# Kernel tuning notes

Hardware: AMD Instinct MI355X
Metric: run time of the kernel (lower is better)

The kernel has to match this reference:

```python
import jax, jax.numpy as jnp
import numpy as np

CHANNELS = [64, 128, 256, 512, 512]
RES = [256, 128, 64, 32, 16]
N = 8          # batch
NQ = 128       # n_quad
NCW = 128      # nc_w (output descriptor size)
GRAD_BOOST = 10.0


def _norm(x):
    # Norm module: per-sample, per-row normalization over last dim; torch std is unbiased (ddof=1)
    m = jnp.mean(x, axis=-1, keepdims=True)
    s = jnp.std(x, axis=-1, ddof=1, keepdims=True)
    return (x - m) / (s + 1e-8)


def _quad(x, w):
    # Quad_module: (M^T @ softmax(grad_boost*w, axis=0))**2, summed over spatial dim
    n, c, h, wd = x.shape
    M = x.reshape(n, c, h * wd)                      # (N, C, HW)
    sm = jax.nn.softmax(w * GRAD_BOOST, axis=0)      # (C, NQ)
    proj = jnp.einsum('nch,co->nho', M, sm)          # (N, HW, NQ)
    return jnp.sum(proj ** 2, axis=1)                # (N, NQ)


def setup_inputs() -> dict:
    key = jax.random.key(0)
    ks = jax.random.split(key, 20)
    inp = {}
    for i, (c, r) in enumerate(zip(CHANNELS, RES)):
        inp[f"x{i}"] = jax.random.normal(ks[i], (N, c, r, r), dtype=jnp.float32)
        # torch init: 5/grad_boost * rand(n_in, n_out) = 0.5 * U[0,1)
        inp[f"w1_{i}"] = 0.5 * jax.random.uniform(ks[5 + i], (c, NQ), dtype=jnp.float32)
    d_in = len(CHANNELS) * NQ
    inp["fc1_w"] = jax.random.normal(ks[10], (d_in, 512), dtype=jnp.float32) * 0.04
    inp["fc1_b"] = jnp.zeros((512,), dtype=jnp.float32)
    inp["fc2_w"] = jax.random.normal(ks[11], (512, 512), dtype=jnp.float32) * 0.04
    inp["fc2_b"] = jnp.zeros((512,), dtype=jnp.float32)
    inp["fc3_w"] = jax.random.normal(ks[12], (512, NCW), dtype=jnp.float32) * 0.04
    inp["fc3_b"] = jnp.zeros((NCW,), dtype=jnp.float32)
    return inp


def reference(x0, x1, x2, x3, x4, w1_0, w1_1, w1_2, w1_3, w1_4,
              fc1_w, fc1_b, fc2_w, fc2_b, fc3_w, fc3_b):
    xs = [x0, x1, x2, x3, x4]
    ws = [w1_0, w1_1, w1_2, w1_3, w1_4]
    feats = [_norm(_quad(x, w)) for x, w in zip(xs, ws)]  # each (N, NQ)
    h = jnp.concatenate(feats, axis=1)                    # (N, 5*NQ)
    h = jax.nn.leaky_relu(_norm(h @ fc1_w + fc1_b), 0.01)
    h = jax.nn.leaky_relu(_norm(h @ fc2_w + fc2_b), 0.01)
    return h @ fc3_w + fc3_b                              # (N, NCW)
```

## Files before the change

### kernel.cpp

```cpp
#include <hip/hip_runtime.h>
#include <hip/hip_bf16.h>
#include <stdint.h>

#define NQ 128
#define NLVL 5

typedef float  floatx4 __attribute__((ext_vector_type(4)));
typedef short  short8  __attribute__((ext_vector_type(8)));

__device__ __forceinline__ uint16_t f2bf(float f) {
    uint32_t u = __builtin_bit_cast(uint32_t, f);
    uint32_t r = u + 0x7FFFu + ((u >> 16) & 1u);
    return (uint16_t)(r >> 16);
}
__device__ __forceinline__ uint32_t pack2(float a, float b) {
    return (uint32_t)f2bf(a) | ((uint32_t)f2bf(b) << 16);
}
__device__ __forceinline__ float bf2f(uint16_t u) {
    return __builtin_bit_cast(float, (uint32_t)u << 16);
}

struct SmParams {
    const float* w[NLVL];
    uint16_t*    smT[NLVL];
    int          C[NLVL];
};

__global__ __launch_bounds__(64) void softmax_kernel(SmParams p) {
    int b   = blockIdx.x;
    int lvl = b >> 7;
    int o   = b & 127;
    int C   = p.C[lvl];
    const float* w = p.w[lvl];
    int lane = threadIdx.x;
    float ev[8];
    int nIter = C >> 6;
    float mx = -1e30f;
    for (int it = 0; it < nIter; ++it) {
        float z = 10.0f * w[(size_t)(it * 64 + lane) * NQ + o];
        ev[it] = z;
        mx = fmaxf(mx, z);
    }
    #pragma unroll
    for (int s = 32; s; s >>= 1) mx = fmaxf(mx, __shfl_xor(mx, s));
    float sum = 0.f;
    for (int it = 0; it < nIter; ++it) { ev[it] = expf(ev[it] - mx); sum += ev[it]; }
    #pragma unroll
    for (int s = 32; s; s >>= 1) sum += __shfl_xor(sum, s);
    float inv = 1.0f / sum;
    uint16_t* dst = p.smT[lvl] + (size_t)o * C;
    for (int it = 0; it < nIter; ++it) dst[it * 64 + lane] = f2bf(ev[it] * inv);
}

struct GramParams { const float* x0; const float* x1; float* g0; float* g1; };

template<int C, int HW, int NS>
__device__ __forceinline__ void gram_body(const float* __restrict__ xb,
                                          float* __restrict__ gb,
                                          int h0, short* lds) {
    constexpr int RF   = C / 64;
    constexpr int CF   = C / 16;
    constexpr int PASS = C / 16;
    constexpr int STR  = 72;

    int t    = threadIdx.x;
    int wv   = t >> 6, lane = t & 63, m = lane & 15, kg = lane >> 4;
    int rrow = t >> 4;
    int rcol = (t & 15) * 4;
    const float* src = xb + (size_t)rrow * HW + rcol + h0;

    floatx4 acc[RF][CF];
    floatx4 zero = {0.f, 0.f, 0.f, 0.f};
    #pragma unroll
    for (int rf = 0; rf < RF; ++rf)
        #pragma unroll
        for (int cf = 0; cf < CF; ++cf) acc[rf][cf] = zero;

    float4 pf[PASS];
    #pragma unroll
    for (int p = 0; p < PASS; ++p) pf[p] = *(const float4*)(src + (size_t)p * 16 * HW);
    #pragma unroll
    for (int p = 0; p < PASS; ++p) {
        uint2 pk = { pack2(pf[p].x, pf[p].y), pack2(pf[p].z, pf[p].w) };
        *(uint2*)&lds[(p * 16 + rrow) * STR + rcol] = pk;
    }

    int cur = 0;
    for (int s = 0; s < NS; ++s) {
        if (s + 1 < NS) {
            const float* s2 = src + (s + 1) * 64;
            #pragma unroll
            for (int p = 0; p < PASS; ++p) pf[p] = *(const float4*)(s2 + (size_t)p * 16 * HW);
        }
        __syncthreads();
        const short* bc = lds + cur * (C * STR);
        #pragma unroll
        for (int ksl = 0; ksl < 2; ++ksl) {
            short8 fr[CF], af[RF];
            #pragma unroll
            for (int f = 0; f < CF; ++f)
                fr[f] = *(const short8*)&bc[(f * 16 + m) * STR + ksl * 32 + kg * 8];
            #pragma unroll
            for (int rf = 0; rf < RF; ++rf)
                af[rf] = *(const short8*)&bc[((wv * RF + rf) * 16 + m) * STR + ksl * 32 + kg * 8];
            #pragma unroll
            for (int rf = 0; rf < RF; ++rf)
                #pragma unroll
                for (int cf = 0; cf < CF; ++cf)
                    acc[rf][cf] = __builtin_amdgcn_mfma_f32_16x16x32_bf16(
                        af[rf], fr[cf], acc[rf][cf], 0, 0, 0);
        }
        if (s + 1 < NS) {
            short* bn = lds + (cur ^ 1) * (C * STR);
            #pragma unroll
            for (int p = 0; p < PASS; ++p) {
                uint2 pk = { pack2(pf[p].x, pf[p].y), pack2(pf[p].z, pf[p].w) };
                *(uint2*)&bn[(p * 16 + rrow) * STR + rcol] = pk;
            }
        }
        cur ^= 1;
    }

    #pragma unroll
    for (int rf = 0; rf < RF; ++rf) {
        int row0 = (wv * RF + rf) * 16 + kg * 4;
        #pragma unroll
        for (int cf = 0; cf < CF; ++cf) {
            int col = cf * 16 + m;
            #pragma unroll
            for (int r = 0; r < 4; ++r)
                atomicAdd(&gb[(size_t)(row0 + r) * C + col], acc[rf][cf][r]);
        }
    }
}

__global__ __launch_bounds__(256) void gram_kernel(GramParams p) {
    __shared__ __align__(16) short lds[2 * 128 * 72];
    int b = blockIdx.x;
    if (b < 512) {
        int n = b >> 6, ch = b & 63;
        gram_body<64, 65536, 16>(p.x0 + (size_t)n * 64 * 65536,
                                 p.g0 + (size_t)n * 64 * 64, ch * 1024, lds);
    } else {
        int b2 = b - 512;
        int n = b2 >> 5, ch = b2 & 31;
        gram_body<128, 16384, 8>(p.x1 + (size_t)n * 128 * 16384,
                                 p.g1 + (size_t)n * 128 * 128, ch * 512, lds);
    }
}

struct SgsParams {
    const float* g0; const float* g1;
    const uint16_t* smT0; const uint16_t* smT1;
    float* quad;
};

template<int C>
__device__ __forceinline__ void sgs_body(const float* __restrict__ g,
                                         const uint16_t* __restrict__ smT,
                                         float* __restrict__ qdst, short* Gt) {
    constexpr int RF  = C / 64;
    constexpr int KSL = C / 32;
    constexpr int STR = C + 8;
    int t = threadIdx.x;
    short* Ghi = Gt;
    short* Glo = Gt + C * STR;
    for (int i = t; i < C * C / 4; i += 256) {
        int row = i / (C / 4);
        int c4  = (i % (C / 4)) * 4;
        float4 v = *(const float4*)(g + (size_t)row * C + c4);
        uint16_t h0 = f2bf(v.x), h1 = f2bf(v.y), h2 = f2bf(v.z), h3 = f2bf(v.w);
        uint2 ph = { (uint32_t)h0 | ((uint32_t)h1 << 16),
                     (uint32_t)h2 | ((uint32_t)h3 << 16) };
        uint2 pl = { pack2(v.x - bf2f(h0), v.y - bf2f(h1)),
                     pack2(v.z - bf2f(h2), v.w - bf2f(h3)) };
        *(uint2*)&Ghi[row * STR + c4] = ph;
        *(uint2*)&Glo[row * STR + c4] = pl;
    }
    __syncthreads();
    int wv = t >> 6, lane = t & 63, m = lane & 15, kg = lane >> 4;
    floatx4 acc[RF][8];
    floatx4 zero = {0.f, 0.f, 0.f, 0.f};
    #pragma unroll
    for (int rf = 0; rf < RF; ++rf)
        #pragma unroll
        for (int ot = 0; ot < 8; ++ot) acc[rf][ot] = zero;

    #pragma unroll
    for (int ksl = 0; ksl < KSL; ++ksl) {
        short8 bf[8];
        #pragma unroll
        for (int ot = 0; ot < 8; ++ot)
            bf[ot] = *(const short8*)(smT + (size_t)(ot * 16 + m) * C + ksl * 32 + kg * 8);
        #pragma unroll
        for (int rf = 0; rf < RF; ++rf) {
            int roff = ((wv * RF + rf) * 16 + m) * STR + ksl * 32 + kg * 8;
            short8 ah = *(const short8*)&Ghi[roff];
            short8 al = *(const short8*)&Glo[roff];
            #pragma unroll
            for (int ot = 0; ot < 8; ++ot) {
                acc[rf][ot] = __builtin_amdgcn_mfma_f32_16x16x32_bf16(ah, bf[ot], acc[rf][ot], 0, 0, 0);
                acc[rf][ot] = __builtin_amdgcn_mfma_f32_16x16x32_bf16(al, bf[ot], acc[rf][ot], 0, 0, 0);
            }
        }
    }
    #pragma unroll
    for (int ot = 0; ot < 8; ++ot) {
        float part = 0.f;
        #pragma unroll
        for (int rf = 0; rf < RF; ++rf) {
            int c0 = (wv * RF + rf) * 16 + kg * 4;
            #pragma unroll
            for (int r = 0; r < 4; ++r) {
                float sv = bf2f(smT[(size_t)(ot * 16 + m) * C + c0 + r]);
                part = fmaf(sv, acc[rf][ot][r], part);
            }
        }
        part += __shfl_xor(part, 16);
        part += __shfl_xor(part, 32);
        if (lane < 16) atomicAdd(qdst + (size_t)(ot * 16 + lane) * 16, part);
    }
}

__global__ __launch_bounds__(256) void sgs_kernel(SgsParams p) {
    __shared__ __align__(16) short Gt[2 * 128 * 136];
    int b = blockIdx.x, lvl = b >> 3, n = b & 7;
    if (lvl == 0)
        sgs_body<64>(p.g0 + (size_t)n * 64 * 64, p.smT0,
                     p.quad + (size_t)n * 128 * 16, Gt);
    else
        sgs_body<128>(p.g1 + (size_t)n * 128 * 128, p.smT1,
                      p.quad + (size_t)(8 + n) * 128 * 16, Gt);
}

struct QuadParams {
    const float*    x[NLVL];
    const uint16_t* smT[NLVL];
    float*          quad;
    int             C[NLVL];
    int             HW[NLVL];
    int             blk_base[NLVL];
};

__global__ __launch_bounds__(256) void quad_kernel(QuadParams p) {
    __shared__ __align__(16) short At[64 * 40];
    __shared__ __align__(16) short Bt[128 * 40];

    int bid = blockIdx.x;
    int lvl = 0;
    #pragma unroll
    for (int l = 1; l < 3; ++l) if (bid >= p.blk_base[l]) lvl = l;
    int rel = bid - p.blk_base[lvl];
    int n   = rel & 7;
    int ht  = rel >> 3;
    int C   = p.C[lvl];
    int HW  = p.HW[lvl];
    int h0  = ht * 64;

    const float*    xb  = p.x[lvl] + (size_t)n * C * HW + h0;
    const uint16_t* smT = p.smT[lvl];

    int t    = threadIdx.x;
    int wave = t >> 6;
    int lane = t & 63;
    int m    = lane & 15;
    int kg   = lane >> 4;

    floatx4 acc[4][2];
    floatx4 zero = {0.f, 0.f, 0.f, 0.f};
    #pragma unroll
    for (int i = 0; i < 4; ++i)
        #pragma unroll
        for (int j = 0; j < 2; ++j) acc[i][j] = zero;

    int c_l = (t & 15) * 2;
    int h_l = (t >> 4) * 4;

    for (int c0 = 0; c0 < C; c0 += 32) {
        const float* s1 = xb + (size_t)(c0 + c_l) * HW + h_l;
        float4 a4 = *(const float4*)s1;
        float4 b4 = *(const float4*)(s1 + HW);
        #pragma unroll
        for (int j = 0; j < 4; ++j) {
            uint32_t pk = (uint32_t)f2bf(((const float*)&a4)[j]) |
                          ((uint32_t)f2bf(((const float*)&b4)[j]) << 16);
            *(uint32_t*)&At[(h_l + j) * 40 + c_l] = pk;
        }
        #pragma unroll
        for (int it = 0; it < 2; ++it) {
            int idx  = it * 256 + t;
            int o    = idx >> 2;
            int part = idx & 3;
            uint4 v = *(const uint4*)(smT + (size_t)o * C + c0 + part * 8);
            *(uint4*)&Bt[o * 40 + part * 8] = v;
        }
        __syncthreads();

        short8 af[4];
        #pragma unroll
        for (int mt = 0; mt < 4; ++mt)
            af[mt] = *(const short8*)&At[(mt * 16 + m) * 40 + kg * 8];
        short8 bfr[2];
        #pragma unroll
        for (int ot = 0; ot < 2; ++ot)
            bfr[ot] = *(const short8*)&Bt[((wave * 2 + ot) * 16 + m) * 40 + kg * 8];
        #pragma unroll
        for (int mt = 0; mt < 4; ++mt)
            #pragma unroll
            for (int ot = 0; ot < 2; ++ot)
                acc[mt][ot] = __builtin_amdgcn_mfma_f32_16x16x32_bf16(
                    af[mt], bfr[ot], acc[mt][ot], 0, 0, 0);
        __syncthreads();
    }

    float* qbase = p.quad + (size_t)((lvl + 2) * 8 + n) * 128 * 16;
    #pragma unroll
    for (int ot = 0; ot < 2; ++ot) {
        float part = 0.f;
        #pragma unroll
        for (int mt = 0; mt < 4; ++mt)
            #pragma unroll
            for (int r = 0; r < 4; ++r) {
                float v = acc[mt][ot][r];
                part = fmaf(v, v, part);
            }
        part += __shfl_xor(part, 16);
        part += __shfl_xor(part, 32);
        if (lane < 16) {
            int o = (wave * 2 + ot) * 16 + lane;
            atomicAdd(qbase + (size_t)o * 16, part);
        }
    }
}


__global__ __launch_bounds__(256) void hfc1_kernel(
    const float* __restrict__ quad, const float* __restrict__ w,
    const float* __restrict__ b, float* __restrict__ h1) {
    __shared__ float feat[640];
    __shared__ float stats[10];
    __shared__ float part[256];
    int blk = blockIdx.x;
    int n = blk >> 3, c8 = blk & 7;
    int t = threadIdx.x;
    for (int idx = t; idx < 640; idx += 256) {
        int L = idx >> 7, o = idx & 127;
        feat[idx] = quad[((size_t)(L * 8 + n) * 128 + o) * 16];
    }
    __syncthreads();
    int wv = t >> 6, lane = t & 63;
    for (int L = wv; L < 5; L += 4) {
        float a = feat[L * 128 + lane], c = feat[L * 128 + 64 + lane];
        float s = a + c;
        #pragma unroll
        for (int sh = 32; sh; sh >>= 1) s += __shfl_xor(s, sh);
        float mean = s * (1.f / 128.f);
        float d0 = a - mean, d1 = c - mean;
        float v = d0 * d0 + d1 * d1;
        #pragma unroll
        for (int sh = 32; sh; sh >>= 1) v += __shfl_xor(v, sh);
        if (lane == 0) {
            stats[L]     = mean;
            stats[5 + L] = 1.f / (sqrtf(v * (1.f / 127.f)) + 1e-8f);
        }
    }
    __syncthreads();
    for (int idx = t; idx < 640; idx += 256) {
        int L = idx >> 7;
        feat[idx] = (feat[idx] - stats[L]) * stats[5 + L];
    }
    __syncthreads();

    int o = c8 * 64 + lane;
    float acc = 0.f;
    const float* wc = w + o;
    int k0 = wv * 160;
    #pragma unroll 8
    for (int k = k0; k < k0 + 160; ++k) acc = fmaf(feat[k], wc[(size_t)k * 512], acc);
    part[t] = acc;
    __syncthreads();
    if (t < 64) {
        float r = part[t] + part[t + 64] + part[t + 128] + part[t + 192];
        h1[(size_t)n * 512 + c8 * 64 + t] = r + b[c8 * 64 + t];
    }
}

__device__ __forceinline__ void norm_leaky_512(float* buf, float* red, int t) {
    float a = buf[t], c = buf[t + 256];
    float s = a + c;
    #pragma unroll
    for (int sh = 32; sh; sh >>= 1) s += __shfl_xor(s, sh);
    if ((t & 63) == 0) red[t >> 6] = s;
    __syncthreads();
    float mean = (red[0] + red[1] + red[2] + red[3]) * (1.f / 512.f);
    float d0 = a - mean, d1 = c - mean;
    float v = d0 * d0 + d1 * d1;
    #pragma unroll
    for (int sh = 32; sh; sh >>= 1) v += __shfl_xor(v, sh);
    __syncthreads();
    if ((t & 63) == 0) red[t >> 6] = v;
    __syncthreads();
    float inv = 1.f / (sqrtf((red[0] + red[1] + red[2] + red[3]) * (1.f / 511.f)) + 1e-8f);
    float n0 = d0 * inv, n1 = d1 * inv;
    buf[t]       = n0 > 0.f ? n0 : 0.01f * n0;
    buf[t + 256] = n1 > 0.f ? n1 : 0.01f * n1;
    __syncthreads();
}

__global__ __launch_bounds__(256) void hfc2_kernel(
    const float* __restrict__ h1, const float* __restrict__ w,
    const float* __restrict__ b, float* __restrict__ h2) {
    __shared__ float buf[512];
    __shared__ float red[4];
    __shared__ float part[256];
    int blk = blockIdx.x;
    int n = blk >> 3, c8 = blk & 7;
    int t = threadIdx.x;
    buf[t]       = h1[(size_t)n * 512 + t];
    buf[t + 256] = h1[(size_t)n * 512 + t + 256];
    __syncthreads();
    norm_leaky_512(buf, red, t);
    int wv = t >> 6, lane = t & 63;
    int o = c8 * 64 + lane;
    float acc = 0.f;
    const float* wc = w + o;
    int k0 = wv * 128;
    #pragma unroll 8
    for (int k = k0; k < k0 + 128; ++k) acc = fmaf(buf[k], wc[(size_t)k * 512], acc);
    part[t] = acc;
    __syncthreads();
    if (t < 64) {
        float r = part[t] + part[t + 64] + part[t + 128] + part[t + 192];
        h2[(size_t)n * 512 + c8 * 64 + t] = r + b[c8 * 64 + t];
    }
}

__global__ __launch_bounds__(256) void hfc3_kernel(
    const float* __restrict__ h2, const float* __restrict__ w,
    const float* __restrict__ b, float* __restrict__ out) {
    __shared__ float buf[512];
    __shared__ float red[4];
    __shared__ float part[256];
    int blk = blockIdx.x;
    int n = blk >> 1, c2 = blk & 1;
    int t = threadIdx.x;
    buf[t]       = h2[(size_t)n * 512 + t];
    buf[t + 256] = h2[(size_t)n * 512 + t + 256];
    __syncthreads();
    norm_leaky_512(buf, red, t);
    int wv = t >> 6, lane = t & 63;
    int o = c2 * 64 + lane;
    float acc = 0.f;
    const float* wc = w + o;
    int k0 = wv * 128;
    #pragma unroll 8
    for (int k = k0; k < k0 + 128; ++k) acc = fmaf(buf[k], wc[(size_t)k * 128], acc);
    part[t] = acc;
    __syncthreads();
    if (t < 64) {
        out[(size_t)n * 128 + c2 * 64 + t] =
            part[t] + part[t + 64] + part[t + 128] + part[t + 192] + b[c2 * 64 + t];
    }
}

extern "C" void kernel_launch(void* const* d_in, const int* in_sizes, int n_in,
                              void* d_out, int out_size, void* d_ws, size_t ws_size,
                              hipStream_t stream) {
    static const int Cs[NLVL]   = {64, 128, 256, 512, 512};
    static const int RESs[NLVL] = {256, 128, 64, 32, 16};

    const float* x[NLVL];
    const float* w[NLVL];
    for (int i = 0; i < NLVL; ++i) {
        x[i] = (const float*)d_in[2 * i];
        w[i] = (const float*)d_in[2 * i + 1];
    }
    const float* fc1_w = (const float*)d_in[10];
    const float* fc1_b = (const float*)d_in[11];
    const float* fc2_w = (const float*)d_in[12];
    const float* fc2_b = (const float*)d_in[13];
    const float* fc3_w = (const float*)d_in[14];
    const float* fc3_b = (const float*)d_in[15];

    uint16_t* smT_base = (uint16_t*)d_ws;
    int smOff[NLVL];
    int off = 0;
    for (int i = 0; i < NLVL; ++i) { smOff[i] = off; off += Cs[i] * NQ; }
    size_t smBytes = (size_t)off * sizeof(uint16_t);
    float* quad = (float*)((char*)d_ws + smBytes);
    size_t quadFloats = (size_t)NLVL * 8 * NQ * 16;
    float* g0 = quad + quadFloats;
    float* g1 = g0 + (size_t)8 * 64 * 64;
    float* h1 = g1 + (size_t)8 * 128 * 128;
    float* h2 = h1 + (size_t)8 * 512;
    size_t zeroBytes = (quadFloats + (size_t)8 * 64 * 64 + (size_t)8 * 128 * 128) * sizeof(float);

    SmParams sp;
    for (int i = 0; i < NLVL; ++i) {
        sp.w[i]   = w[i];
        sp.smT[i] = smT_base + smOff[i];
        sp.C[i]   = Cs[i];
    }
    softmax_kernel<<<NLVL * NQ, 64, 0, stream>>>(sp);

    hipMemsetAsync(quad, 0, zeroBytes, stream);

    GramParams gp;
    gp.x0 = x[0]; gp.x1 = x[1]; gp.g0 = g0; gp.g1 = g1;
    gram_kernel<<<768, 256, 0, stream>>>(gp);

    QuadParams qp;
    int base = 0;
    for (int i = 0; i < 3; ++i) {
        int lvl = i + 2;
        qp.x[i]   = x[lvl];
        qp.smT[i] = smT_base + smOff[lvl];
        qp.C[i]   = Cs[lvl];
        qp.HW[i]  = RESs[lvl] * RESs[lvl];
        qp.blk_base[i] = base;
        base += (RESs[lvl] * RESs[lvl] / 64) * 8;
    }
    for (int i = 3; i < NLVL; ++i) {
        qp.x[i] = nullptr; qp.smT[i] = nullptr;
        qp.C[i] = 0; qp.HW[i] = 0; qp.blk_base[i] = 0x7fffffff;
    }
    qp.quad = quad;
    quad_kernel<<<base, 256, 0, stream>>>(qp);

    SgsParams ssp;
    ssp.g0 = g0; ssp.g1 = g1;
    ssp.smT0 = smT_base + smOff[0];
    ssp.smT1 = smT_base + smOff[1];
    ssp.quad = quad;
    sgs_kernel<<<16, 256, 0, stream>>>(ssp);

    hfc1_kernel<<<64, 256, 0, stream>>>(quad, fc1_w, fc1_b, h1);
    hfc2_kernel<<<64, 256, 0, stream>>>(h1, fc2_w, fc2_b, h2);
    hfc3_kernel<<<16, 256, 0, stream>>>(h2, fc3_w, fc3_b, (float*)d_out);
}
```

Before: 391.1 us.

## Fuse softmax into Gram kernel and SGS into quad kernel, direct-load Gram tiles

```diff
diff --git a/kernel.cpp b/kernel.cpp
--- a/kernel.cpp
+++ b/kernel.cpp
@@ -19,165 +19,217 @@
 __device__ __forceinline__ float bf2f(uint16_t u) {
     return __builtin_bit_cast(float, (uint32_t)u << 16);
 }
-
-struct SmParams {
+__device__ __forceinline__ short8 cvt8(float4 lo, float4 hi) {
+    union { short8 s; uint32_t u[4]; } r;
+    r.u[0] = pack2(lo.x, lo.y);
+    r.u[1] = pack2(lo.z, lo.w);
+    r.u[2] = pack2(hi.x, hi.y);
+    r.u[3] = pack2(hi.z, hi.w);
+    return r.s;
+}
+__device__ __forceinline__ void split_hilo(float4 v0, float4 v1, short8& hi, short8& lo) {
+    hi = cvt8(v0, v1);
+    float4 r0, r1;
+    r0.x = v0.x - bf2f((uint16_t)hi[0]); r0.y = v0.y - bf2f((uint16_t)hi[1]);
+    r0.z = v0.z - bf2f((uint16_t)hi[2]); r0.w = v0.w - bf2f((uint16_t)hi[3]);
+    r1.x = v1.x - bf2f((uint16_t)hi[4]); r1.y = v1.y - bf2f((uint16_t)hi[5]);
+    r1.z = v1.z - bf2f((uint16_t)hi[6]); r1.w = v1.w - bf2f((uint16_t)hi[7]);
+    lo = cvt8(r0, r1);
+}
+
+#define MFMA16(a, b, c) __builtin_amdgcn_mfma_f32_16x16x32_bf16((a), (b), (c), 0, 0, 0)
+
+
+struct AParams {
+    const float* x0; const float* x1;
+    float*       g0; float*       g1;
     const float* w[NLVL];
     uint16_t*    smT[NLVL];
     int          C[NLVL];
 };
 
-__global__ __launch_bounds__(64) void softmax_kernel(SmParams p) {
-    int b   = blockIdx.x;
-    int lvl = b >> 7;
-    int o   = b & 127;
-    int C   = p.C[lvl];
-    const float* w = p.w[lvl];
-    int lane = threadIdx.x;
-    float ev[8];
-    int nIter = C >> 6;
-    float mx = -1e30f;
-    for (int it = 0; it < nIter; ++it) {
-        float z = 10.0f * w[(size_t)(it * 64 + lane) * NQ + o];
-        ev[it] = z;
-        mx = fmaxf(mx, z);
-    }
-    #pragma unroll
-    for (int s = 32; s; s >>= 1) mx = fmaxf(mx, __shfl_xor(mx, s));
-    float sum = 0.f;
-    for (int it = 0; it < nIter; ++it) { ev[it] = expf(ev[it] - mx); sum += ev[it]; }
-    #pragma unroll
-    for (int s = 32; s; s >>= 1) sum += __shfl_xor(sum, s);
-    float inv = 1.0f / sum;
-    uint16_t* dst = p.smT[lvl] + (size_t)o * C;
-    for (int it = 0; it < nIter; ++it) dst[it * 64 + lane] = f2bf(ev[it] * inv);
-}
-
-struct GramParams { const float* x0; const float* x1; float* g0; float* g1; };
-
-template<int C, int HW, int NS>
-__device__ __forceinline__ void gram_body(const float* __restrict__ xb,
-                                          float* __restrict__ gb,
-                                          int h0, short* lds) {
-    constexpr int RF   = C / 64;
-    constexpr int CF   = C / 16;
-    constexpr int PASS = C / 16;
-    constexpr int STR  = 72;
-
-    int t    = threadIdx.x;
-    int wv   = t >> 6, lane = t & 63, m = lane & 15, kg = lane >> 4;
-    int rrow = t >> 4;
-    int rcol = (t & 15) * 4;
-    const float* src = xb + (size_t)rrow * HW + rcol + h0;
-
-    floatx4 acc[RF][CF];
+__device__ __forceinline__ void gram_tile_diag(
+    const float* __restrict__ base, int ldr, int k0, int nst,
+    int m, int kg, floatx4 (&acc)[4][4])
+{
+    float4 Alo[4], Ahi[4], Blo[4], Bhi[4];
+    {
+        int k = k0 + kg * 8;
+        #pragma unroll
+        for (int f = 0; f < 4; ++f) {
+            const float* q = base + (size_t)(f * 16 + m) * ldr + k;
+            Alo[f] = *(const float4*)q; Ahi[f] = *(const float4*)(q + 4);
+        }
+    }
+    for (int s = 0; s < nst; s += 2) {
+        if (s + 1 < nst) {
+            int k1 = k0 + (s + 1) * 32 + kg * 8;
+            #pragma unroll
+            for (int f = 0; f < 4; ++f) {
+                const float* q = base + (size_t)(f * 16 + m) * ldr + k1;
+                Blo[f] = *(const float4*)q; Bhi[f] = *(const float4*)(q + 4);
+            }
+        }
+        {
+            short8 fr[4];
+            #pragma unroll
+            for (int f = 0; f < 4; ++f) fr[f] = cvt8(Alo[f], Ahi[f]);
+            #pragma unroll
+            for (int rf = 0; rf < 4; ++rf)
+                #pragma unroll
+                for (int cf = 0; cf < 4; ++cf)
+                    acc[rf][cf] = MFMA16(fr[rf], fr[cf], acc[rf][cf]);
+        }
+        if (s + 2 < nst) {
+            int k2 = k0 + (s + 2) * 32 + kg * 8;
+            #pragma unroll
+            for (int f = 0; f < 4; ++f) {
+                const float* q = base + (size_t)(f * 16 + m) * ldr + k2;
+                Alo[f] = *(const float4*)q; Ahi[f] = *(const float4*)(q + 4);
+            }
+        }
+        if (s + 1 < nst) {
+            short8 fr[4];
+            #pragma unroll
+            for (int f = 0; f < 4; ++f) fr[f] = cvt8(Blo[f], Bhi[f]);
+            #pragma unroll
+            for (int rf = 0; rf < 4; ++rf)
+                #pragma unroll
+                for (int cf = 0; cf < 4; ++cf)
+                    acc[rf][cf] = MFMA16(fr[rf], fr[cf], acc[rf][cf]);
+        }
+    }
+}
+
+__device__ __forceinline__ void gram_tile_off(
+    const float* __restrict__ ab, const float* __restrict__ bb,
+    int ldr, int k0, int nst, int m, int kg, floatx4 (&acc)[4][4])
+{
+    #pragma unroll 2
+    for (int s = 0; s < nst; ++s) {
+        int k = k0 + s * 32 + kg * 8;
+        float4 a0[4], a1[4], b0[4], b1[4];
+        #pragma unroll
+        for (int f = 0; f < 4; ++f) {
+            const float* qa = ab + (size_t)(f * 16 + m) * ldr + k;
+            const float* qb = bb + (size_t)(f * 16 + m) * ldr + k;
+            a0[f] = *(const float4*)qa; a1[f] = *(const float4*)(qa + 4);
+            b0[f] = *(const float4*)qb; b1[f] = *(const float4*)(qb + 4);
+        }
+        short8 af[4], bf[4];
+        #pragma unroll
+        for (int f = 0; f < 4; ++f) {
+            af[f] = cvt8(a0[f], a1[f]);
+            bf[f] = cvt8(b0[f], b1[f]);
+        }
+        #pragma unroll
+        for (int rf = 0; rf < 4; ++rf)
+            #pragma unroll
+            for (int cf = 0; cf < 4; ++cf)
+                acc[rf][cf] = MFMA16(af[rf], bf[cf], acc[rf][cf]);
+    }
+}
+
+__global__ __launch_bounds__(256) void gram_sm_kernel(AParams p) {
+    __shared__ float gred[4096];
+    int b  = blockIdx.x;
+    int t  = threadIdx.x;
+    int wv = t >> 6, lane = t & 63, m = lane & 15, kg = lane >> 4;
+
+    if (b >= 320) {
+        int idx = (b - 320) * 4 + wv;
+        int lvl = idx >> 7, o = idx & 127;
+        int C   = p.C[lvl];
+        const float* w = p.w[lvl];
+        float ev[8];
+        int nIter = C >> 6;
+        float mx = -1e30f;
+        for (int it = 0; it < nIter; ++it) {
+            float z = 10.0f * w[(size_t)(it * 64 + lane) * NQ + o];
+            ev[it] = z;
+            mx = fmaxf(mx, z);
+        }
+        #pragma unroll
+        for (int s = 32; s; s >>= 1) mx = fmaxf(mx, __shfl_xor(mx, s));
+        float sum = 0.f;
+        for (int it = 0; it < nIter; ++it) { ev[it] = expf(ev[it] - mx); sum += ev[it]; }
+        #pragma unroll
+        for (int s = 32; s; s >>= 1) sum += __shfl_xor(sum, s);
+        float inv = 1.0f / sum;
+        uint16_t* dst = p.smT[lvl] + (size_t)o * C;
+        for (int it = 0; it < nIter; ++it) dst[it * 64 + lane] = f2bf(ev[it] * inv);
+        return;
+    }
+
+    floatx4 acc[4][4];
     floatx4 zero = {0.f, 0.f, 0.f, 0.f};
     #pragma unroll
-    for (int rf = 0; rf < RF; ++rf)
-        #pragma unroll
-        for (int cf = 0; cf < CF; ++cf) acc[rf][cf] = zero;
-
-    float4 pf[PASS];
-    #pragma unroll
-    for (int p = 0; p < PASS; ++p) pf[p] = *(const float4*)(src + (size_t)p * 16 * HW);
-    #pragma unroll
-    for (int p = 0; p < PASS; ++p) {
-        uint2 pk = { pack2(pf[p].x, pf[p].y), pack2(pf[p].z, pf[p].w) };
-        *(uint2*)&lds[(p * 16 + rrow) * STR + rcol] = pk;
-    }
-
-    int cur = 0;
-    for (int s = 0; s < NS; ++s) {
-        if (s + 1 < NS) {
-            const float* s2 = src + (s + 1) * 64;
-            #pragma unroll
-            for (int p = 0; p < PASS; ++p) pf[p] = *(const float4*)(s2 + (size_t)p * 16 * HW);
-        }
+    for (int i = 0; i < 4; ++i)
+        #pragma unroll
+        for (int j = 0; j < 4; ++j) acc[i][j] = zero;
+
+    if (b < 256) {
+        int n = b >> 5, ch = b & 31;
+        const float* xb = p.x0 + (size_t)n * 64 * 65536;
+        int k0 = ch * 2048 + wv * 512;
+        gram_tile_diag(xb, 65536, k0, 16, m, kg, acc);
+
+        for (int i = t; i < 4096; i += 256) gred[i] = 0.f;
         __syncthreads();
-        const short* bc = lds + cur * (C * STR);
-        #pragma unroll
-        for (int ksl = 0; ksl < 2; ++ksl) {
-            short8 fr[CF], af[RF];
-            #pragma unroll
-            for (int f = 0; f < CF; ++f)
-                fr[f] = *(const short8*)&bc[(f * 16 + m) * STR + ksl * 32 + kg * 8];
-            #pragma unroll
-            for (int rf = 0; rf < RF; ++rf)
-                af[rf] = *(const short8*)&bc[((wv * RF + rf) * 16 + m) * STR + ksl * 32 + kg * 8];
-            #pragma unroll
-            for (int rf = 0; rf < RF; ++rf)
+        #pragma unroll
+        for (int rf = 0; rf < 4; ++rf)
+            #pragma unroll
+            for (int cf = 0; cf < 4; ++cf)
                 #pragma unroll
-                for (int cf = 0; cf < CF; ++cf)
-                    acc[rf][cf] = __builtin_amdgcn_mfma_f32_16x16x32_bf16(
-                        af[rf], fr[cf], acc[rf][cf], 0, 0, 0);
-        }
-        if (s + 1 < NS) {
-            short* bn = lds + (cur ^ 1) * (C * STR);
-            #pragma unroll
-            for (int p = 0; p < PASS; ++p) {
-                uint2 pk = { pack2(pf[p].x, pf[p].y), pack2(pf[p].z, pf[p].w) };
-                *(uint2*)&bn[(p * 16 + rrow) * STR + rcol] = pk;
-            }
-        }
-        cur ^= 1;
-    }
-
-    #pragma unroll
-    for (int rf = 0; rf < RF; ++rf) {
-        int row0 = (wv * RF + rf) * 16 + kg * 4;
-        #pragma unroll
-        for (int cf = 0; cf < CF; ++cf) {
-            int col = cf * 16 + m;
-            #pragma unroll
-            for (int r = 0; r < 4; ++r)
-                atomicAdd(&gb[(size_t)(row0 + r) * C + col], acc[rf][cf][r]);
-        }
-    }
-}
-
-__global__ __launch_bounds__(256) void gram_kernel(GramParams p) {
-    __shared__ __align__(16) short lds[2 * 128 * 72];
-    int b = blockIdx.x;
-    if (b < 512) {
-        int n = b >> 6, ch = b & 63;
-        gram_body<64, 65536, 16>(p.x0 + (size_t)n * 64 * 65536,
-                                 p.g0 + (size_t)n * 64 * 64, ch * 1024, lds);
+                for (int r = 0; r < 4; ++r)
+                    atomicAdd(&gred[(rf * 16 + kg * 4 + r) * 64 + cf * 16 + m],
+                              acc[rf][cf][r]);
+        __syncthreads();
+        float* gb = p.g0 + (size_t)n * 4096;
+        for (int i = t; i < 4096; i += 256) atomicAdd(&gb[i], gred[i]);
     } else {
-        int b2 = b - 512;
-        int n = b2 >> 5, ch = b2 & 31;
-        gram_body<128, 16384, 8>(p.x1 + (size_t)n * 128 * 16384,
-                                 p.g1 + (size_t)n * 128 * 128, ch * 512, lds);
-    }
-}
-
-struct SgsParams {
-    const float* g0; const float* g1;
+        int b2 = b - 256;
+        int n = b2 >> 3, kc = b2 & 7;
+        const float* xb = p.x1 + (size_t)n * 128 * 16384;
+        int rb = wv >> 1, cb = wv & 1;
+        const float* ab = xb + (size_t)rb * 64 * 16384;
+        const float* bb = xb + (size_t)cb * 64 * 16384;
+        int k0 = kc * 2048;
+        if (rb == cb) gram_tile_diag(ab, 16384, k0, 64, m, kg, acc);
+        else          gram_tile_off(ab, bb, 16384, k0, 64, m, kg, acc);
+        float* gb = p.g1 + (size_t)n * 16384;
+        #pragma unroll
+        for (int rf = 0; rf < 4; ++rf)
+            #pragma unroll
+            for (int cf = 0; cf < 4; ++cf)
+                #pragma unroll
+                for (int r = 0; r < 4; ++r)
+                    atomicAdd(&gb[(size_t)(rb * 64 + rf * 16 + kg * 4 + r) * 128 +
+                                  cb * 64 + cf * 16 + m],
+                              acc[rf][cf][r]);
+    }
+}
+
+
+struct QSParams {
+    const float*    x[3];
+    const uint16_t* smT[3];
+    float*          quad;
+    int             C[3];
+    int             HW[3];
+    int             blk_base[3];
+    int             quad_blocks;
+    const float*    g0; const float* g1;
     const uint16_t* smT0; const uint16_t* smT1;
-    float* quad;
 };
 
 template<int C>
-__device__ __forceinline__ void sgs_body(const float* __restrict__ g,
-                                         const uint16_t* __restrict__ smT,
-                                         float* __restrict__ qdst, short* Gt) {
+__device__ __forceinline__ void sgs_direct(const float* __restrict__ g,
+                                           const uint16_t* __restrict__ smT,
+                                           float* __restrict__ qdst) {
     constexpr int RF  = C / 64;
     constexpr int KSL = C / 32;
-    constexpr int STR = C + 8;
     int t = threadIdx.x;
-    short* Ghi = Gt;
-    short* Glo = Gt + C * STR;
-    for (int i = t; i < C * C / 4; i += 256) {
-        int row = i / (C / 4);
-        int c4  = (i % (C / 4)) * 4;
-        float4 v = *(const float4*)(g + (size_t)row * C + c4);
-        uint16_t h0 = f2bf(v.x), h1 = f2bf(v.y), h2 = f2bf(v.z), h3 = f2bf(v.w);
-        uint2 ph = { (uint32_t)h0 | ((uint32_t)h1 << 16),
-                     (uint32_t)h2 | ((uint32_t)h3 << 16) };
-        uint2 pl = { pack2(v.x - bf2f(h0), v.y - bf2f(h1)),
-                     pack2(v.z - bf2f(h2), v.w - bf2f(h3)) };
-        *(uint2*)&Ghi[row * STR + c4] = ph;
-        *(uint2*)&Glo[row * STR + c4] = pl;
-    }
-    __syncthreads();
     int wv = t >> 6, lane = t & 63, m = lane & 15, kg = lane >> 4;
     floatx4 acc[RF][8];
     floatx4 zero = {0.f, 0.f, 0.f, 0.f};
@@ -188,19 +240,20 @@
 
     #pragma unroll
     for (int ksl = 0; ksl < KSL; ++ksl) {
-        short8 bf[8];
+        short8 bfr[8];
         #pragma unroll
         for (int ot = 0; ot < 8; ++ot)
-            bf[ot] = *(const short8*)(smT + (size_t)(ot * 16 + m) * C + ksl * 32 + kg * 8);
+            bfr[ot] = *(const short8*)(smT + (size_t)(ot * 16 + m) * C + ksl * 32 + kg * 8);
         #pragma unroll
         for (int rf = 0; rf < RF; ++rf) {
-            int roff = ((wv * RF + rf) * 16 + m) * STR + ksl * 32 + kg * 8;
-            short8 ah = *(const short8*)&Ghi[roff];
-            short8 al = *(const short8*)&Glo[roff];
+            const float* gp = g + (size_t)((wv * RF + rf) * 16 + m) * C + ksl * 32 + kg * 8;
+            float4 v0 = *(const float4*)gp, v1 = *(const float4*)(gp + 4);
+            short8 ah, al;
+            split_hilo(v0, v1, ah, al);
             #pragma unroll
             for (int ot = 0; ot < 8; ++ot) {
-                acc[rf][ot] = __builtin_amdgcn_mfma_f32_16x16x32_bf16(ah, bf[ot], acc[rf][ot], 0, 0, 0);
-                acc[rf][ot] = __builtin_amdgcn_mfma_f32_16x16x32_bf16(al, bf[ot], acc[rf][ot], 0, 0, 0);
+                acc[rf][ot] = MFMA16(ah, bfr[ot], acc[rf][ot]);
+                acc[rf][ot] = MFMA16(al, bfr[ot], acc[rf][ot]);
             }
         }
     }
@@ -222,31 +275,23 @@
     }
 }
 
-__global__ __launch_bounds__(256) void sgs_kernel(SgsParams p) {
-    __shared__ __align__(16) short Gt[2 * 128 * 136];
-    int b = blockIdx.x, lvl = b >> 3, n = b & 7;
-    if (lvl == 0)
-        sgs_body<64>(p.g0 + (size_t)n * 64 * 64, p.smT0,
-                     p.quad + (size_t)n * 128 * 16, Gt);
-    else
-        sgs_body<128>(p.g1 + (size_t)n * 128 * 128, p.smT1,
-                      p.quad + (size_t)(8 + n) * 128 * 16, Gt);
-}
-
-struct QuadParams {
-    const float*    x[NLVL];
-    const uint16_t* smT[NLVL];
-    float*          quad;
-    int             C[NLVL];
-    int             HW[NLVL];
-    int             blk_base[NLVL];
-};
-
-__global__ __launch_bounds__(256) void quad_kernel(QuadParams p) {
+__global__ __launch_bounds__(256) void quad_sgs_kernel(QSParams p) {
     __shared__ __align__(16) short At[64 * 40];
     __shared__ __align__(16) short Bt[128 * 40];
 
     int bid = blockIdx.x;
+    if (bid >= p.quad_blocks) {
+        int b = bid - p.quad_blocks;
+        int lvl = b >> 3, n = b & 7;
+        if (lvl == 0)
+            sgs_direct<64>(p.g0 + (size_t)n * 4096, p.smT0,
+                           p.quad + (size_t)n * 2048);
+        else
+            sgs_direct<128>(p.g1 + (size_t)n * 16384, p.smT1,
+                            p.quad + (size_t)(8 + n) * 2048);
+        return;
+    }
+
     int lvl = 0;
     #pragma unroll
     for (int l = 1; l < 3; ++l) if (bid >= p.blk_base[l]) lvl = l;
@@ -308,8 +353,7 @@
         for (int mt = 0; mt < 4; ++mt)
             #pragma unroll
             for (int ot = 0; ot < 2; ++ot)
-                acc[mt][ot] = __builtin_amdgcn_mfma_f32_16x16x32_bf16(
-                    af[mt], bfr[ot], acc[mt][ot], 0, 0, 0);
+                acc[mt][ot] = MFMA16(af[mt], bfr[ot], acc[mt][ot]);
         __syncthreads();
     }
 
@@ -332,7 +376,6 @@
         }
     }
 }
-
 
 __global__ __launch_bounds__(256) void hfc1_kernel(
     const float* __restrict__ quad, const float* __restrict__ w,
@@ -371,9 +414,8 @@
     }
     __syncthreads();
 
-    int o = c8 * 64 + lane;
     float acc = 0.f;
-    const float* wc = w + o;
+    const float* wc = w + c8 * 64 + lane;
     int k0 = wv * 160;
     #pragma unroll 8
     for (int k = k0; k < k0 + 160; ++k) acc = fmaf(feat[k], wc[(size_t)k * 512], acc);
@@ -421,9 +463,8 @@
     __syncthreads();
     norm_leaky_512(buf, red, t);
     int wv = t >> 6, lane = t & 63;
-    int o = c8 * 64 + lane;
     float acc = 0.f;
-    const float* wc = w + o;
+    const float* wc = w + c8 * 64 + lane;
     int k0 = wv * 128;
     #pragma unroll 8
     for (int k = k0; k < k0 + 128; ++k) acc = fmaf(buf[k], wc[(size_t)k * 512], acc);
@@ -449,9 +490,8 @@
     __syncthreads();
     norm_leaky_512(buf, red, t);
     int wv = t >> 6, lane = t & 63;
-    int o = c2 * 64 + lane;
     float acc = 0.f;
-    const float* wc = w + o;
+    const float* wc = w + c2 * 64 + lane;
     int k0 = wv * 128;
     #pragma unroll 8
     for (int k = k0; k < k0 + 128; ++k) acc = fmaf(buf[k], wc[(size_t)k * 128], acc);
@@ -495,21 +535,18 @@
     float* h2 = h1 + (size_t)8 * 512;
     size_t zeroBytes = (quadFloats + (size_t)8 * 64 * 64 + (size_t)8 * 128 * 128) * sizeof(float);
 
-    SmParams sp;
+    hipMemsetAsync(quad, 0, zeroBytes, stream);
+
+    AParams ap;
+    ap.x0 = x[0]; ap.x1 = x[1]; ap.g0 = g0; ap.g1 = g1;
     for (int i = 0; i < NLVL; ++i) {
-        sp.w[i]   = w[i];
-        sp.smT[i] = smT_base + smOff[i];
-        sp.C[i]   = Cs[i];
-    }
-    softmax_kernel<<<NLVL * NQ, 64, 0, stream>>>(sp);
-
-    hipMemsetAsync(quad, 0, zeroBytes, stream);
-
-    GramParams gp;
-    gp.x0 = x[0]; gp.x1 = x[1]; gp.g0 = g0; gp.g1 = g1;
-    gram_kernel<<<768, 256, 0, stream>>>(gp);
-
-    QuadParams qp;
+        ap.w[i]   = w[i];
+        ap.smT[i] = smT_base + smOff[i];
+        ap.C[i]   = Cs[i];
+    }
+    gram_sm_kernel<<<480, 256, 0, stream>>>(ap);
+
+    QSParams qp;
     int base = 0;
     for (int i = 0; i < 3; ++i) {
         int lvl = i + 2;
@@ -520,19 +557,12 @@
         qp.blk_base[i] = base;
         base += (RESs[lvl] * RESs[lvl] / 64) * 8;
     }
-    for (int i = 3; i < NLVL; ++i) {
-        qp.x[i] = nullptr; qp.smT[i] = nullptr;
-        qp.C[i] = 0; qp.HW[i] = 0; qp.blk_base[i] = 0x7fffffff;
-    }
     qp.quad = quad;
-    quad_kernel<<<base, 256, 0, stream>>>(qp);
-
-    SgsParams ssp;
-    ssp.g0 = g0; ssp.g1 = g1;
-    ssp.smT0 = smT_base + smOff[0];
-    ssp.smT1 = smT_base + smOff[1];
-    ssp.quad = quad;
-    sgs_kernel<<<16, 256, 0, stream>>>(ssp);
+    qp.quad_blocks = base;
+    qp.g0 = g0; qp.g1 = g1;
+    qp.smT0 = smT_base + smOff[0];
+    qp.smT1 = smT_base + smOff[1];
+    quad_sgs_kernel<<<base + 16, 256, 0, stream>>>(qp);
 
     hfc1_kernel<<<64, 256, 0, stream>>>(quad, fc1_w, fc1_b, h1);
     hfc2_kernel<<<64, 256, 0, stream>>>(h1, fc2_w, fc2_b, h2);
```

Result: slower. 483.6 us (+23.6%).
